# Kernel optimization log

Measured on AMD Instinct MI355X. Metric: run time of the kernel, lower is better.

## Reference

```python
import jax, jax.numpy as jnp
import numpy as np
from jax import lax


def setup_inputs() -> dict:
    key = jax.random.key(0)
    ks = jax.random.split(key, 8)
    B, S, H, L = 64, 512, 768, 9
    hidden = jax.random.normal(ks[0], (B, S, H), jnp.float32)
    label = jax.random.randint(ks[1], (B, S), 0, L, dtype=jnp.int32)
    mask = jnp.ones((B, S), jnp.int32)
    W = jax.random.normal(ks[2], (H, L), jnp.float32) * 0.02
    b = jnp.zeros((L,), jnp.float32)
    start_transitions = jax.random.normal(ks[3], (L,), jnp.float32) * 0.1
    end_transitions = jax.random.normal(ks[4], (L,), jnp.float32) * 0.1
    transitions = jax.random.normal(ks[5], (L, L), jnp.float32) * 0.1
    return dict(hidden=hidden, label=label, mask=mask, W=W, b=b,
                start_transitions=start_transitions,
                end_transitions=end_transitions,
                transitions=transitions)


def reference(hidden, label, mask, W, b, start_transitions, end_transitions, transitions):
    B, S, H = hidden.shape
    L = b.shape[0]
    # output_layer: [B,S,H] @ [H,L] -> emissions, then transpose to time-major [S,B,L]
    emissions = jnp.einsum('bsh,hl->bsl', hidden, W) + b
    em = jnp.transpose(emissions, (1, 0, 2))        # [S, B, L]
    tags = label.T                                   # [S, B]
    m = mask.T.astype(jnp.float32)                   # [S, B]

    def gather_tag(em_t, tag_t):
        # em_t [B,L], tag_t [B] -> [B]
        return jnp.take_along_axis(em_t, tag_t[:, None], axis=1)[:, 0]

    # ---- numerator: score of the gold path ----
    score0 = start_transitions[tags[0]] + gather_tag(em[0], tags[0])
    def num_step(carry, x):
        score, prev = carry
        em_t, tag_t, m_t = x
        s = transitions[prev, tag_t] + gather_tag(em_t, tag_t)
        score = score + s * m_t
        prev = jnp.where(m_t > 0, tag_t, prev)
        return (score, prev), None
    (score, last_gold), _ = lax.scan(num_step, (score0, tags[0]), (em[1:], tags[1:], m[1:]))
    score = score + end_transitions[last_gold]

    # ---- denominator: forward algorithm (logsumexp DP) ----
    alpha0 = start_transitions[None, :] + em[0]      # [B, L]
    def fwd_step(alpha, x):
        em_t, m_t = x
        nxt = jax.nn.logsumexp(alpha[:, :, None] + transitions[None, :, :] + em_t[:, None, :], axis=1)
        alpha = jnp.where(m_t[:, None] > 0, nxt, alpha)
        return alpha, None
    alphaT, _ = lax.scan(fwd_step, alpha0, (em[1:], m[1:]))
    logZ = jax.nn.logsumexp(alphaT + end_transitions[None, :], axis=1)

    llh = jnp.sum(score - logZ)                      # reduction='sum'
    loss = -llh / B

    # ---- Viterbi decode (decode() is called without mask -> full length) ----
    v0 = start_transitions[None, :] + em[0]
    def vit_step(v, em_t):
        scores = v[:, :, None] + transitions[None, :, :] + em_t[:, None, :]  # [B, L, L]
        return jnp.max(scores, axis=1), jnp.argmax(scores, axis=1)
    vT, hist = lax.scan(vit_step, v0, em[1:])        # hist [S-1, B, L]
    last_tag = jnp.argmax(vT + end_transitions[None, :], axis=1)  # [B]
    def back_step(tag, bp_t):
        prev = jnp.take_along_axis(bp_t, tag[:, None], axis=1)[:, 0]
        return prev, prev
    _, prevs = lax.scan(back_step, last_tag, hist, reverse=True)  # [S-1, B]
    path = jnp.concatenate([prevs, last_tag[None, :]], axis=0).T  # [B, S]

    # ---- accuracy bookkeeping (label > 0 mask) ----
    label_flat = label.reshape(-1)
    label_mask = (label_flat > 0).astype(jnp.int32)
    predict = path.reshape(-1).astype(jnp.int32) * label_mask
    correct = jnp.sum((predict == label_flat).astype(jnp.float32))
    return loss, correct, predict, label_flat
```

## Files before the change

kernel.cpp:

```cpp
#include <hip/hip_runtime.h>
#include <hip/hip_bf16.h>

#define NB 64
#define NS 512
#define NH 768
#define NL 9
#define NROWS (NB*NS)
#define EMN (NROWS*NL)

__device__ __forceinline__ float readlane_f(float v, int l) {
    return __int_as_float(__builtin_amdgcn_readlane(__float_as_int(v), l));
}
__device__ __forceinline__ unsigned long long readlane_u64(unsigned long long v, int l) {
    unsigned int lo = (unsigned int)__builtin_amdgcn_readlane((int)(unsigned int)(v & 0xffffffffULL), l);
    unsigned int hi = (unsigned int)__builtin_amdgcn_readlane((int)(unsigned int)(v >> 32), l);
    return ((unsigned long long)hi << 32) | (unsigned long long)lo;
}

__global__ __launch_bounds__(256) void k_gemm_part(const float* __restrict__ hidden,
                                                   const float* __restrict__ W,
                                                   float* __restrict__ part) {
    int bx = blockIdx.x;
    int rb = bx >> 1, ks = bx & 1;
    int row = rb * 256 + threadIdx.x;
    int kbase = ks * (NH / 2);
    const float4* hp = (const float4*)(hidden + (size_t)row * NH + kbase);
    float acc[NL];
#pragma unroll
    for (int j = 0; j < NL; j++) acc[j] = 0.f;
#pragma unroll 4
    for (int c = 0; c < NH / 2 / 4; c++) {
        float4 h = hp[c];
        int k0 = kbase + 4 * c;
#pragma unroll
        for (int j = 0; j < NL; j++) {
            acc[j] = fmaf(h.x, W[(k0 + 0) * NL + j], acc[j]);
            acc[j] = fmaf(h.y, W[(k0 + 1) * NL + j], acc[j]);
            acc[j] = fmaf(h.z, W[(k0 + 2) * NL + j], acc[j]);
            acc[j] = fmaf(h.w, W[(k0 + 3) * NL + j], acc[j]);
        }
    }
    float* o = part + (size_t)ks * EMN + (size_t)row * NL;
#pragma unroll
    for (int j = 0; j < NL; j++) o[j] = acc[j];
}

__global__ __launch_bounds__(256) void k_combine(const float* __restrict__ part,
                                                 const float* __restrict__ bias,
                                                 float* __restrict__ em,
                                                 float* __restrict__ out) {
    int idx = blockIdx.x * 256 + threadIdx.x;
    float v = bias[idx % NL] + part[idx] + part[EMN + idx];
    em[idx] = v;
    if (idx == 0) { out[0] = 0.f; out[1] = 0.f; }
}

__global__ __launch_bounds__(64) void k_dp(const float* __restrict__ em,
                                           const int* __restrict__ label,
                                           const int* __restrict__ mask,
                                           const float* __restrict__ startT,
                                           const float* __restrict__ endT,
                                           const float* __restrict__ trans,
                                           float* __restrict__ logZ,
                                           float* __restrict__ score,
                                           unsigned char* __restrict__ path) {
    __shared__ unsigned char bp[NS * NL];
    __shared__ float Tlds[NL * NL];
    int bx = blockIdx.x;
    int lane = threadIdx.x;
    int j = lane;
    int j9 = j < NL ? j : NL - 1;

    if (bx < NB) {
        int b = bx;
        const float* eb = em + (size_t)b * NS * NL;
        const int* mb = mask + b * NS;
        float Mcol[NL];
#pragma unroll
        for (int i = 0; i < NL; i++) Mcol[i] = __expf(trans[i * NL + j9]);
        float a = __expf(startT[j9] + eb[j9]);
        float logacc = 0.f;
        float epre[4]; int mpre[4];
#pragma unroll
        for (int p = 0; p < 4; p++) { int tt = 1 + p; epre[p] = eb[tt * NL + j9]; mpre[p] = mb[tt]; }
#pragma unroll 4
        for (int t = 1; t < NS; ++t) {
            float emv = epre[0]; int mv = mpre[0];
            epre[0] = epre[1]; epre[1] = epre[2]; epre[2] = epre[3];
            mpre[0] = mpre[1]; mpre[1] = mpre[2]; mpre[2] = mpre[3];
            int tn = t + 4; tn = tn < NS ? tn : NS - 1;
            epre[3] = eb[tn * NL + j9]; mpre[3] = mb[tn];
            float s = 0.f;
#pragma unroll
            for (int i = 0; i < NL; i++) s = fmaf(readlane_f(a, i), Mcol[i], s);
            float anew = __expf(emv) * s;
            a = (mv > 0) ? anew : a;
            if ((t & 7) == 0) {
                float c = 0.f;
#pragma unroll
                for (int i = 0; i < NL; i++) c += readlane_f(a, i);
                a = a / c;
                logacc += __logf(c);
            }
        }
        float z = a * __expf(endT[j9]);
        float c = 0.f;
#pragma unroll
        for (int i = 0; i < NL; i++) c += readlane_f(z, i);
        if (lane == 0) logZ[b] = logacc + __logf(c);
    } else if (bx < 2 * NB) {
        int b = bx - NB;
        const float* eb = em + (size_t)b * NS * NL;
        float Tcol[NL];
#pragma unroll
        for (int i = 0; i < NL; i++) Tcol[i] = trans[i * NL + j9];
        float v = startT[j9] + eb[j9];
        if (j < NL) bp[j] = (unsigned char)j;
        float epre[4];
#pragma unroll
        for (int p = 0; p < 4; p++) epre[p] = eb[(1 + p) * NL + j9];
#pragma unroll 4
        for (int t = 1; t < NS; ++t) {
            float emv = epre[0];
            epre[0] = epre[1]; epre[1] = epre[2]; epre[2] = epre[3];
            int tn = t + 4; tn = tn < NS ? tn : NS - 1;
            epre[3] = eb[tn * NL + j9];
            float best = (readlane_f(v, 0) + Tcol[0]) + emv;
            int bi = 0;
#pragma unroll
            for (int i = 1; i < NL; i++) {
                float val = (readlane_f(v, i) + Tcol[i]) + emv;
                bool g = val > best;
                best = g ? val : best;
                bi = g ? i : bi;
            }
            v = best;
            if (j < NL) bp[t * NL + j] = (unsigned char)bi;
        }
        __syncthreads();
        float f = v + endT[j9];
        int lt = 0;
        float bb = readlane_f(f, 0);
#pragma unroll
        for (int jj = 1; jj < NL; jj++) {
            float fj = readlane_f(f, jj);
            if (fj > bb) { bb = fj; lt = jj; }
        }
        unsigned long long G[8];
#pragma unroll
        for (int r = 0; r < 8; r++) {
            int t0 = (lane * 8 + r) * NL;
            unsigned long long g = 0;
#pragma unroll
            for (int x = 0; x < NL; x++) g |= (unsigned long long)bp[t0 + x] << (4 * x);
            G[r] = g;
        }
        unsigned long long A = 0x876543210ULL;
#pragma unroll
        for (int r = 7; r >= 0; r--) {
            unsigned long long An = 0;
#pragma unroll
            for (int x = 0; x < NL; x++) {
                int ax = (int)((A >> (4 * x)) & 15ULL);
                int gv = (int)((G[r] >> (4 * ax)) & 15ULL);
                An |= (unsigned long long)gv << (4 * x);
            }
            A = An;
        }
        int e = 0; int cur = lt;
        for (int ll = 63; ll >= 0; --ll) {
            if (lane == ll) e = cur;
            unsigned long long Al = readlane_u64(A, ll);
            cur = (int)((Al >> (4 * cur)) & 15ULL);
        }
        unsigned long long pw = 0; int c2 = e;
#pragma unroll
        for (int r = 7; r >= 0; r--) {
            pw |= (unsigned long long)c2 << (8 * r);
            c2 = (int)((G[r] >> (4 * c2)) & 15ULL);
        }
        *(unsigned long long*)(path + (size_t)b * NS + lane * 8) = pw;
    } else {
        int b = bx - 2 * NB;
        for (int q = lane; q < NL * NL; q += 64) Tlds[q] = trans[q];
        __syncthreads();
        const float* eb = em + (size_t)b * NS * NL;
        const int* lb = label + b * NS;
        const int* mb = mask + b * NS;
        int t0 = lane * 8;
        int lab[8]; int mk[8];
#pragma unroll
        for (int r = 0; r < 8; r++) { lab[r] = lb[t0 + r]; mk[r] = mb[t0 + r]; }
        if (lane == 0) mk[0] = 1;
        int h = 0, sl = 0;
#pragma unroll
        for (int r = 0; r < 8; r++) { if (mk[r] > 0) { h = 1; sl = lab[r]; } }
#pragma unroll
        for (int d = 1; d < 64; d <<= 1) {
            int ho = __shfl_up(h, d);
            int so = __shfl_up(sl, d);
            if (!h) { h = ho; sl = so; }
        }
        int lg = __shfl(sl, 63);
        int incoming = __shfl_up(sl, 1);
        float sc = 0.f;
        int prevr = (lane == 0) ? lab[0] : incoming;
#pragma unroll
        for (int r = 0; r < 8; r++) {
            int t = t0 + r;
            if (t > 0) {
                float s = Tlds[prevr * NL + lab[r]] + eb[t * NL + lab[r]];
                sc += s * (float)mk[r];
            }
            if (mk[r] > 0) prevr = lab[r];
        }
        if (lane == 0) {
            int g0 = lab[0];
            sc += startT[g0] + eb[g0] + endT[lg];
        }
#pragma unroll
        for (int d = 1; d < 64; d <<= 1) sc += __shfl_xor(sc, d);
        if (lane == 0) score[b] = sc;
    }
}

__global__ __launch_bounds__(256) void k_fin(const int* __restrict__ label,
                                             const unsigned char* __restrict__ path,
                                             const float* __restrict__ logZ,
                                             const float* __restrict__ score,
                                             float* __restrict__ out) {
    int b = blockIdx.x;
    int tid = threadIdx.x;
    float cnt = 0.f;
#pragma unroll
    for (int q = 0; q < 2; q++) {
        int t = tid + q * 256;
        int idx = b * NS + t;
        int lab = label[idx];
        int p = (int)path[idx];
        int pred = (lab > 0) ? p : 0;
        out[2 + idx] = (float)pred;
        out[2 + NROWS + idx] = (float)lab;
        cnt += (pred == lab) ? 1.f : 0.f;
    }
#pragma unroll
    for (int d = 1; d < 64; d <<= 1) cnt += __shfl_xor(cnt, d);
    if ((tid & 63) == 0) atomicAdd(out + 1, cnt);
    if (b == 0 && tid < 64) {
        float dsc = score[tid] - logZ[tid];
#pragma unroll
        for (int d = 1; d < 64; d <<= 1) dsc += __shfl_xor(dsc, d);
        if (tid == 0) out[0] = -dsc / (float)NB;
    }
}

extern "C" void kernel_launch(void* const* d_in, const int* in_sizes, int n_in,
                              void* d_out, int out_size, void* d_ws, size_t ws_size,
                              hipStream_t stream) {
    const float* hidden = (const float*)d_in[0];
    const int*   label  = (const int*)d_in[1];
    const int*   mask   = (const int*)d_in[2];
    const float* W      = (const float*)d_in[3];
    const float* bias   = (const float*)d_in[4];
    const float* startT = (const float*)d_in[5];
    const float* endT   = (const float*)d_in[6];
    const float* trans  = (const float*)d_in[7];
    float* out = (float*)d_out;

    float* ws    = (float*)d_ws;
    float* em    = ws;
    float* part  = ws + EMN;
    float* logZv = part;
    float* scorev = part + 64;
    unsigned char* path = (unsigned char*)(part + 128);

    k_gemm_part<<<256, 256, 0, stream>>>(hidden, W, part);
    k_combine<<<1152, 256, 0, stream>>>(part, bias, em, out);
    k_dp<<<192, 64, 0, stream>>>(em, label, mask, startT, endT, trans, logZv, scorev, path);
    k_fin<<<64, 256, 0, stream>>>(label, path, logZv, scorev, out);
}
```

Before: 259.1 us.

## Fuse GEMM with bias, stage emissions in LDS, parallelize Viterbi backpointers

The GEMM now assigns one wavefront per four rows, keeps W in registers, reduces across lanes with shuffles and adds the bias in the same kernel, so the separate combine kernel and the partial-sum buffer are gone. The DP kernel runs 256 threads per block and first copies each batch's emissions and mask into LDS. The Viterbi recurrence keeps only the max on its serial path and stores the scores. Backpointer argmaxes are then recomputed in parallel across all threads, and forward-algorithm normalization uses exponent extraction with ldexp instead of a divide and log. This shortens the serial per-step chain and removes launches and memory traffic, at the cost of large shared-memory use per block and idle threads during the serial phases.

```diff
diff --git a/kernel.cpp b/kernel.cpp
--- a/kernel.cpp
+++ b/kernel.cpp
@@ -17,210 +17,284 @@
     return ((unsigned long long)hi << 32) | (unsigned long long)lo;
 }
 
-__global__ __launch_bounds__(256) void k_gemm_part(const float* __restrict__ hidden,
-                                                   const float* __restrict__ W,
-                                                   float* __restrict__ part) {
+__global__ __launch_bounds__(256) void k_gemm(const float* __restrict__ hidden,
+                                              const float* __restrict__ W,
+                                              const float* __restrict__ bias,
+                                              float* __restrict__ em,
+                                              float* __restrict__ out) {
+    int tid = threadIdx.x;
+    int lane = tid & 63;
+    int w = blockIdx.x * 4 + (tid >> 6);
+    if (blockIdx.x == 0 && tid == 0) { out[0] = 0.f; out[1] = 0.f; }
+
+    float4 Wr[3][9];
+    const float4* Wp = (const float4*)W;
+#pragma unroll
+    for (int c = 0; c < 3; c++) {
+        const float4* p = Wp + 9 * lane + 576 * c;
+#pragma unroll
+        for (int q = 0; q < 9; q++) Wr[c][q] = p[q];
+    }
+    float bz[NL];
+#pragma unroll
+    for (int j = 0; j < NL; j++) bz[j] = bias[j];
+
+#pragma unroll
+    for (int r = 0; r < 4; r++) {
+        int row = 4 * w + r;
+        const float* hp = hidden + (size_t)row * NH;
+        float4 h[3];
+#pragma unroll
+        for (int c = 0; c < 3; c++) h[c] = *(const float4*)(hp + 4 * lane + 256 * c);
+        float acc[NL];
+#pragma unroll
+        for (int j = 0; j < NL; j++) acc[j] = 0.f;
+#pragma unroll
+        for (int c = 0; c < 3; c++) {
+            const float hv[4] = { h[c].x, h[c].y, h[c].z, h[c].w };
+#pragma unroll
+            for (int kk = 0; kk < 4; kk++) {
+#pragma unroll
+                for (int j = 0; j < NL; j++) {
+                    int fl = kk * 9 + j;
+                    const float4& wq = Wr[c][fl >> 2];
+                    float wv = (fl & 3) == 0 ? wq.x : (fl & 3) == 1 ? wq.y : (fl & 3) == 2 ? wq.z : wq.w;
+                    acc[j] = fmaf(hv[kk], wv, acc[j]);
+                }
+            }
+        }
+#pragma unroll
+        for (int m = 1; m < 64; m <<= 1) {
+#pragma unroll
+            for (int j = 0; j < NL; j++) acc[j] += __shfl_xor(acc[j], m);
+        }
+        if (lane == 0) {
+            float* o = em + (size_t)row * NL;
+#pragma unroll
+            for (int j = 0; j < NL; j++) o[j] = acc[j] + bz[j];
+        }
+    }
+}
+
+__global__ __launch_bounds__(256) void k_dp(const float* __restrict__ em,
+                                            const int* __restrict__ label,
+                                            const int* __restrict__ mask,
+                                            const float* __restrict__ startT,
+                                            const float* __restrict__ endT,
+                                            const float* __restrict__ trans,
+                                            float* __restrict__ logZ,
+                                            float* __restrict__ score,
+                                            unsigned char* __restrict__ path) {
+    __shared__ float s_em[NS * NL];
+    __shared__ float s_v[NS * NL];
+    __shared__ unsigned char s_bp[NS * NL];
+    __shared__ int s_mk[NS];
+    __shared__ float s_T[NL * NL];
+
     int bx = blockIdx.x;
-    int rb = bx >> 1, ks = bx & 1;
-    int row = rb * 256 + threadIdx.x;
-    int kbase = ks * (NH / 2);
-    const float4* hp = (const float4*)(hidden + (size_t)row * NH + kbase);
-    float acc[NL];
-#pragma unroll
-    for (int j = 0; j < NL; j++) acc[j] = 0.f;
+    int tid = threadIdx.x;
+    int role = bx >> 6;
+    int b = bx & 63;
+
+    {
+        const float4* ef = (const float4*)(em + (size_t)b * NS * NL);
+        float4* sf = (float4*)s_em;
+        for (int q = tid; q < NS * NL / 4; q += 256) sf[q] = ef[q];
+        if (tid < NS / 4) ((int4*)s_mk)[tid] = ((const int4*)(mask + b * NS))[tid];
+        if (tid < NL * NL) s_T[tid] = trans[tid];
+    }
+    __syncthreads();
+
+    if (role == 0) {
+        if (tid < 64) {
+            int j9 = tid < NL ? tid : NL - 1;
+            float Mcol[NL];
+#pragma unroll
+            for (int i = 0; i < NL; i++) Mcol[i] = __expf(s_T[i * NL + j9]);
+            float a = __expf(startT[j9] + s_em[j9]);
+            int eacc = 0;
+            float epre[4]; int mpre[4];
+#pragma unroll
+            for (int p = 0; p < 4; p++) { epre[p] = s_em[(1 + p) * NL + j9]; mpre[p] = s_mk[1 + p]; }
 #pragma unroll 4
-    for (int c = 0; c < NH / 2 / 4; c++) {
-        float4 h = hp[c];
-        int k0 = kbase + 4 * c;
-#pragma unroll
-        for (int j = 0; j < NL; j++) {
-            acc[j] = fmaf(h.x, W[(k0 + 0) * NL + j], acc[j]);
-            acc[j] = fmaf(h.y, W[(k0 + 1) * NL + j], acc[j]);
-            acc[j] = fmaf(h.z, W[(k0 + 2) * NL + j], acc[j]);
-            acc[j] = fmaf(h.w, W[(k0 + 3) * NL + j], acc[j]);
-        }
-    }
-    float* o = part + (size_t)ks * EMN + (size_t)row * NL;
-#pragma unroll
-    for (int j = 0; j < NL; j++) o[j] = acc[j];
-}
-
-__global__ __launch_bounds__(256) void k_combine(const float* __restrict__ part,
-                                                 const float* __restrict__ bias,
-                                                 float* __restrict__ em,
-                                                 float* __restrict__ out) {
-    int idx = blockIdx.x * 256 + threadIdx.x;
-    float v = bias[idx % NL] + part[idx] + part[EMN + idx];
-    em[idx] = v;
-    if (idx == 0) { out[0] = 0.f; out[1] = 0.f; }
-}
-
-__global__ __launch_bounds__(64) void k_dp(const float* __restrict__ em,
-                                           const int* __restrict__ label,
-                                           const int* __restrict__ mask,
-                                           const float* __restrict__ startT,
-                                           const float* __restrict__ endT,
-                                           const float* __restrict__ trans,
-                                           float* __restrict__ logZ,
-                                           float* __restrict__ score,
-                                           unsigned char* __restrict__ path) {
-    __shared__ unsigned char bp[NS * NL];
-    __shared__ float Tlds[NL * NL];
-    int bx = blockIdx.x;
-    int lane = threadIdx.x;
-    int j = lane;
-    int j9 = j < NL ? j : NL - 1;
-
-    if (bx < NB) {
-        int b = bx;
-        const float* eb = em + (size_t)b * NS * NL;
-        const int* mb = mask + b * NS;
-        float Mcol[NL];
-#pragma unroll
-        for (int i = 0; i < NL; i++) Mcol[i] = __expf(trans[i * NL + j9]);
-        float a = __expf(startT[j9] + eb[j9]);
-        float logacc = 0.f;
-        float epre[4]; int mpre[4];
-#pragma unroll
-        for (int p = 0; p < 4; p++) { int tt = 1 + p; epre[p] = eb[tt * NL + j9]; mpre[p] = mb[tt]; }
+            for (int t = 1; t < NS; ++t) {
+                float emv = epre[0]; int mv = mpre[0];
+                epre[0] = epre[1]; epre[1] = epre[2]; epre[2] = epre[3];
+                mpre[0] = mpre[1]; mpre[1] = mpre[2]; mpre[2] = mpre[3];
+                int tn = t + 4; tn = tn < NS ? tn : NS - 1;
+                epre[3] = s_em[tn * NL + j9]; mpre[3] = s_mk[tn];
+                float p0 = readlane_f(a, 0) * Mcol[0];
+                float p1 = readlane_f(a, 1) * Mcol[1];
+                float p2 = readlane_f(a, 2) * Mcol[2];
+                float p3 = readlane_f(a, 3) * Mcol[3];
+                float p4 = readlane_f(a, 4) * Mcol[4];
+                float p5 = readlane_f(a, 5) * Mcol[5];
+                float p6 = readlane_f(a, 6) * Mcol[6];
+                float p7 = readlane_f(a, 7) * Mcol[7];
+                float p8 = readlane_f(a, 8) * Mcol[8];
+                float s = (((p0 + p1) + (p2 + p3)) + ((p4 + p5) + (p6 + p7))) + p8;
+                float anew = __expf(emv) * s;
+                a = (mv > 0) ? anew : a;
+                if ((t & 7) == 0) {
+                    float c0 = readlane_f(a, 0), c1 = readlane_f(a, 1), c2 = readlane_f(a, 2);
+                    float c3 = readlane_f(a, 3), c4 = readlane_f(a, 4), c5 = readlane_f(a, 5);
+                    float c6 = readlane_f(a, 6), c7 = readlane_f(a, 7), c8 = readlane_f(a, 8);
+                    float c = (((c0 + c1) + (c2 + c3)) + ((c4 + c5) + (c6 + c7))) + c8;
+                    int ex = ((__float_as_int(c) >> 23) & 255) - 127;
+                    a = ldexpf(a, -ex);
+                    eacc += ex;
+                }
+            }
+            float z = a * __expf(endT[j9]);
+            float c0 = readlane_f(z, 0), c1 = readlane_f(z, 1), c2 = readlane_f(z, 2);
+            float c3 = readlane_f(z, 3), c4 = readlane_f(z, 4), c5 = readlane_f(z, 5);
+            float c6 = readlane_f(z, 6), c7 = readlane_f(z, 7), c8 = readlane_f(z, 8);
+            float c = (((c0 + c1) + (c2 + c3)) + ((c4 + c5) + (c6 + c7))) + c8;
+            if (tid == 0) logZ[b] = (float)eacc * 0.6931471805599453f + __logf(c);
+        }
+    } else if (role == 1) {
+        if (tid < 64) {
+            int j9 = tid < NL ? tid : NL - 1;
+            float Tcol[NL];
+#pragma unroll
+            for (int i = 0; i < NL; i++) Tcol[i] = s_T[i * NL + j9];
+            float v = startT[j9] + s_em[j9];
+            if (tid < NL) { s_v[tid] = v; s_bp[tid] = (unsigned char)tid; }
+            float epre[4];
+#pragma unroll
+            for (int p = 0; p < 4; p++) epre[p] = s_em[(1 + p) * NL + j9];
 #pragma unroll 4
-        for (int t = 1; t < NS; ++t) {
-            float emv = epre[0]; int mv = mpre[0];
-            epre[0] = epre[1]; epre[1] = epre[2]; epre[2] = epre[3];
-            mpre[0] = mpre[1]; mpre[1] = mpre[2]; mpre[2] = mpre[3];
-            int tn = t + 4; tn = tn < NS ? tn : NS - 1;
-            epre[3] = eb[tn * NL + j9]; mpre[3] = mb[tn];
-            float s = 0.f;
-#pragma unroll
-            for (int i = 0; i < NL; i++) s = fmaf(readlane_f(a, i), Mcol[i], s);
-            float anew = __expf(emv) * s;
-            a = (mv > 0) ? anew : a;
-            if ((t & 7) == 0) {
-                float c = 0.f;
-#pragma unroll
-                for (int i = 0; i < NL; i++) c += readlane_f(a, i);
-                a = a / c;
-                logacc += __logf(c);
-            }
-        }
-        float z = a * __expf(endT[j9]);
-        float c = 0.f;
-#pragma unroll
-        for (int i = 0; i < NL; i++) c += readlane_f(z, i);
-        if (lane == 0) logZ[b] = logacc + __logf(c);
-    } else if (bx < 2 * NB) {
-        int b = bx - NB;
-        const float* eb = em + (size_t)b * NS * NL;
-        float Tcol[NL];
-#pragma unroll
-        for (int i = 0; i < NL; i++) Tcol[i] = trans[i * NL + j9];
-        float v = startT[j9] + eb[j9];
-        if (j < NL) bp[j] = (unsigned char)j;
-        float epre[4];
-#pragma unroll
-        for (int p = 0; p < 4; p++) epre[p] = eb[(1 + p) * NL + j9];
-#pragma unroll 4
-        for (int t = 1; t < NS; ++t) {
-            float emv = epre[0];
-            epre[0] = epre[1]; epre[1] = epre[2]; epre[2] = epre[3];
-            int tn = t + 4; tn = tn < NS ? tn : NS - 1;
-            epre[3] = eb[tn * NL + j9];
-            float best = (readlane_f(v, 0) + Tcol[0]) + emv;
-            int bi = 0;
-#pragma unroll
-            for (int i = 1; i < NL; i++) {
-                float val = (readlane_f(v, i) + Tcol[i]) + emv;
-                bool g = val > best;
-                best = g ? val : best;
-                bi = g ? i : bi;
-            }
-            v = best;
-            if (j < NL) bp[t * NL + j] = (unsigned char)bi;
+            for (int t = 1; t < NS; ++t) {
+                float emv = epre[0];
+                epre[0] = epre[1]; epre[1] = epre[2]; epre[2] = epre[3];
+                int tn = t + 4; tn = tn < NS ? tn : NS - 1;
+                epre[3] = s_em[tn * NL + j9];
+                float m0 = readlane_f(v, 0) + Tcol[0];
+                float m1 = readlane_f(v, 1) + Tcol[1];
+                float m2 = readlane_f(v, 2) + Tcol[2];
+                float m3 = readlane_f(v, 3) + Tcol[3];
+                float m4 = readlane_f(v, 4) + Tcol[4];
+                float m5 = readlane_f(v, 5) + Tcol[5];
+                float m6 = readlane_f(v, 6) + Tcol[6];
+                float m7 = readlane_f(v, 7) + Tcol[7];
+                float m8 = readlane_f(v, 8) + Tcol[8];
+                float M = fmaxf(fmaxf(fmaxf(fmaxf(m0, m1), fmaxf(m2, m3)),
+                                      fmaxf(fmaxf(m4, m5), fmaxf(m6, m7))), m8);
+                v = M + emv;
+                if (tid < NL) s_v[t * NL + tid] = v;
+            }
         }
         __syncthreads();
-        float f = v + endT[j9];
-        int lt = 0;
-        float bb = readlane_f(f, 0);
-#pragma unroll
-        for (int jj = 1; jj < NL; jj++) {
-            float fj = readlane_f(f, jj);
-            if (fj > bb) { bb = fj; lt = jj; }
-        }
-        unsigned long long G[8];
-#pragma unroll
-        for (int r = 0; r < 8; r++) {
-            int t0 = (lane * 8 + r) * NL;
-            unsigned long long g = 0;
-#pragma unroll
-            for (int x = 0; x < NL; x++) g |= (unsigned long long)bp[t0 + x] << (4 * x);
-            G[r] = g;
-        }
-        unsigned long long A = 0x876543210ULL;
-#pragma unroll
-        for (int r = 7; r >= 0; r--) {
-            unsigned long long An = 0;
-#pragma unroll
-            for (int x = 0; x < NL; x++) {
-                int ax = (int)((A >> (4 * x)) & 15ULL);
-                int gv = (int)((G[r] >> (4 * ax)) & 15ULL);
-                An |= (unsigned long long)gv << (4 * x);
-            }
-            A = An;
-        }
-        int e = 0; int cur = lt;
-        for (int ll = 63; ll >= 0; --ll) {
-            if (lane == ll) e = cur;
-            unsigned long long Al = readlane_u64(A, ll);
-            cur = (int)((Al >> (4 * cur)) & 15ULL);
-        }
-        unsigned long long pw = 0; int c2 = e;
-#pragma unroll
-        for (int r = 7; r >= 0; r--) {
-            pw |= (unsigned long long)c2 << (8 * r);
-            c2 = (int)((G[r] >> (4 * c2)) & 15ULL);
-        }
-        *(unsigned long long*)(path + (size_t)b * NS + lane * 8) = pw;
+#pragma unroll
+        for (int rep = 0; rep < 2; rep++) {
+            int t = 1 + tid + 256 * rep;
+            if (t < NS) {
+                float vp[NL], emt[NL];
+#pragma unroll
+                for (int i = 0; i < NL; i++) vp[i] = s_v[(t - 1) * NL + i];
+#pragma unroll
+                for (int j = 0; j < NL; j++) emt[j] = s_em[t * NL + j];
+#pragma unroll
+                for (int j = 0; j < NL; j++) {
+                    float e = emt[j];
+                    float val[NL];
+#pragma unroll
+                    for (int i = 0; i < NL; i++) val[i] = (vp[i] + s_T[i * NL + j]) + e;
+                    bool c01 = val[0] >= val[1]; float m01 = c01 ? val[0] : val[1]; int i01 = c01 ? 0 : 1;
+                    bool c23 = val[2] >= val[3]; float m23 = c23 ? val[2] : val[3]; int i23 = c23 ? 2 : 3;
+                    bool c45 = val[4] >= val[5]; float m45 = c45 ? val[4] : val[5]; int i45 = c45 ? 4 : 5;
+                    bool c67 = val[6] >= val[7]; float m67 = c67 ? val[6] : val[7]; int i67 = c67 ? 6 : 7;
+                    bool ca = m01 >= m23; float ma = ca ? m01 : m23; int ia = ca ? i01 : i23;
+                    bool cb = m45 >= m67; float mb = cb ? m45 : m67; int ib = cb ? i45 : i67;
+                    bool cc = ma >= mb;  float mc = cc ? ma : mb;  int ic = cc ? ia : ib;
+                    bool cd = mc >= val[8]; int bi = cd ? ic : 8;
+                    s_bp[t * NL + j] = (unsigned char)bi;
+                }
+            }
+        }
+        __syncthreads();
+        if (tid < 64) {
+            int lane = tid;
+            float bb = s_v[(NS - 1) * NL + 0] + endT[0]; int lt = 0;
+#pragma unroll
+            for (int jj = 1; jj < NL; jj++) {
+                float fj = s_v[(NS - 1) * NL + jj] + endT[jj];
+                if (fj > bb) { bb = fj; lt = jj; }
+            }
+            unsigned long long G[8];
+#pragma unroll
+            for (int r = 0; r < 8; r++) {
+                int t0 = (lane * 8 + r) * NL;
+                unsigned long long g = 0;
+#pragma unroll
+                for (int x = 0; x < NL; x++) g |= (unsigned long long)s_bp[t0 + x] << (4 * x);
+                G[r] = g;
+            }
+            unsigned long long A = 0x876543210ULL;
+#pragma unroll
+            for (int r = 7; r >= 0; r--) {
+                unsigned long long An = 0;
+#pragma unroll
+                for (int x = 0; x < NL; x++) {
+                    int ax = (int)((A >> (4 * x)) & 15ULL);
+                    int gv = (int)((G[r] >> (4 * ax)) & 15ULL);
+                    An |= (unsigned long long)gv << (4 * x);
+                }
+                A = An;
+            }
+            int e = 0; int cur = lt;
+            for (int ll = 63; ll >= 0; --ll) {
+                if (lane == ll) e = cur;
+                unsigned long long Al = readlane_u64(A, ll);
+                cur = (int)((Al >> (4 * cur)) & 15ULL);
+            }
+            unsigned long long pw = 0; int c2 = e;
+#pragma unroll
+            for (int r = 7; r >= 0; r--) {
+                pw |= (unsigned long long)c2 << (8 * r);
+                c2 = (int)((G[r] >> (4 * c2)) & 15ULL);
+            }
+            *(unsigned long long*)(path + (size_t)b * NS + lane * 8) = pw;
+        }
     } else {
-        int b = bx - 2 * NB;
-        for (int q = lane; q < NL * NL; q += 64) Tlds[q] = trans[q];
-        __syncthreads();
-        const float* eb = em + (size_t)b * NS * NL;
-        const int* lb = label + b * NS;
-        const int* mb = mask + b * NS;
-        int t0 = lane * 8;
-        int lab[8]; int mk[8];
-#pragma unroll
-        for (int r = 0; r < 8; r++) { lab[r] = lb[t0 + r]; mk[r] = mb[t0 + r]; }
-        if (lane == 0) mk[0] = 1;
-        int h = 0, sl = 0;
-#pragma unroll
-        for (int r = 0; r < 8; r++) { if (mk[r] > 0) { h = 1; sl = lab[r]; } }
-#pragma unroll
-        for (int d = 1; d < 64; d <<= 1) {
-            int ho = __shfl_up(h, d);
-            int so = __shfl_up(sl, d);
-            if (!h) { h = ho; sl = so; }
-        }
-        int lg = __shfl(sl, 63);
-        int incoming = __shfl_up(sl, 1);
-        float sc = 0.f;
-        int prevr = (lane == 0) ? lab[0] : incoming;
-#pragma unroll
-        for (int r = 0; r < 8; r++) {
-            int t = t0 + r;
-            if (t > 0) {
-                float s = Tlds[prevr * NL + lab[r]] + eb[t * NL + lab[r]];
-                sc += s * (float)mk[r];
-            }
-            if (mk[r] > 0) prevr = lab[r];
-        }
-        if (lane == 0) {
-            int g0 = lab[0];
-            sc += startT[g0] + eb[g0] + endT[lg];
-        }
-#pragma unroll
-        for (int d = 1; d < 64; d <<= 1) sc += __shfl_xor(sc, d);
-        if (lane == 0) score[b] = sc;
+        if (tid < 64) {
+            int lane = tid;
+            const int* lb = label + b * NS;
+            int t0 = lane * 8;
+            int lab[8]; int mk[8];
+#pragma unroll
+            for (int r = 0; r < 8; r++) { lab[r] = lb[t0 + r]; mk[r] = s_mk[t0 + r]; }
+            if (lane == 0) mk[0] = 1;
+            int h = 0, sl = 0;
+#pragma unroll
+            for (int r = 0; r < 8; r++) { if (mk[r] > 0) { h = 1; sl = lab[r]; } }
+#pragma unroll
+            for (int d = 1; d < 64; d <<= 1) {
+                int ho = __shfl_up(h, d);
+                int so = __shfl_up(sl, d);
+                if (!h) { h = ho; sl = so; }
+            }
+            int lg = __shfl(sl, 63);
+            int incoming = __shfl_up(sl, 1);
+            float sc = 0.f;
+            int prevr = (lane == 0) ? lab[0] : incoming;
+#pragma unroll
+            for (int r = 0; r < 8; r++) {
+                int t = t0 + r;
+                if (t > 0) {
+                    float s = s_T[prevr * NL + lab[r]] + s_em[t * NL + lab[r]];
+                    sc += s * (float)mk[r];
+                }
+                if (mk[r] > 0) prevr = lab[r];
+            }
+            if (lane == 0) {
+                int g0 = lab[0];
+                sc += startT[g0] + s_em[g0] + endT[lg];
+            }
+#pragma unroll
+            for (int d = 1; d < 64; d <<= 1) sc += __shfl_xor(sc, d);
+            if (lane == 0) score[b] = sc;
+        }
     }
 }
 
@@ -267,15 +341,13 @@
     const float* trans  = (const float*)d_in[7];
     float* out = (float*)d_out;
 
-    float* ws    = (float*)d_ws;
-    float* em    = ws;
-    float* part  = ws + EMN;
-    float* logZv = part;
-    float* scorev = part + 64;
-    unsigned char* path = (unsigned char*)(part + 128);
-
-    k_gemm_part<<<256, 256, 0, stream>>>(hidden, W, part);
-    k_combine<<<1152, 256, 0, stream>>>(part, bias, em, out);
-    k_dp<<<192, 64, 0, stream>>>(em, label, mask, startT, endT, trans, logZv, scorev, path);
+    float* ws     = (float*)d_ws;
+    float* em     = ws;
+    float* logZv  = ws + EMN;
+    float* scorev = ws + EMN + 64;
+    unsigned char* path = (unsigned char*)(ws + EMN + 128);
+
+    k_gemm<<<2048, 256, 0, stream>>>(hidden, W, bias, em, out);
+    k_dp<<<192, 256, 0, stream>>>(em, label, mask, startT, endT, trans, logZv, scorev, path);
     k_fin<<<64, 256, 0, stream>>>(label, path, logZv, scorev, out);
 }
```

Result: faster. 219.0 us (-15.5%).
